# Optimization experiments

Hardware: AMD Instinct MI355X
Metric: run time of the kernel (lower is better)

The kernel has to match this reference:

```python
import jax, jax.numpy as jnp
import numpy as np

NHEAD = 16
D_MODEL = 1024
D_K = D_MODEL // NHEAD


def setup_inputs() -> dict:
    key = jax.random.key(0)
    ks = jax.random.split(key, 12)
    B, S, D = 2, 2048, D_MODEL
    scale = 1.0 / np.sqrt(D)
    inp = {
        "value": jax.random.normal(ks[0], (B, S, D), dtype=jnp.float32),
        "key": jax.random.normal(ks[1], (B, S, D), dtype=jnp.float32),
        "query": jax.random.normal(ks[2], (B, S, D), dtype=jnp.float32),
        "mask": jax.random.randint(ks[3], (B, 1, S, S), 0, 2, dtype=jnp.int32),
        "Wv": jax.random.normal(ks[4], (D, D), dtype=jnp.float32) * scale,
        "bv": jnp.zeros((D,), dtype=jnp.float32),
        "Wk": jax.random.normal(ks[5], (D, D), dtype=jnp.float32) * scale,
        "bk": jnp.zeros((D,), dtype=jnp.float32),
        "Wq": jax.random.normal(ks[6], (D, D), dtype=jnp.float32) * scale,
        "bq": jnp.zeros((D,), dtype=jnp.float32),
        "Wo": jax.random.normal(ks[7], (D, D), dtype=jnp.float32) * scale,
        "bo": jnp.zeros((D,), dtype=jnp.float32),
    }
    return inp


def reference(value, key, query, mask, Wv, bv, Wk, bk, Wq, bq, Wo, bo):
    B, S, D = value.shape
    H, Dk = NHEAD, D_K

    def proj(x, W, b):
        # nn.Linear: x @ W^T + b, then split heads -> [B, H, S, Dk]
        return (x @ W.T + b).reshape(B, S, H, Dk).transpose(0, 2, 1, 3)

    v = proj(value, Wv, bv)
    k = proj(key, Wk, bk)
    q = proj(query, Wq, bq)

    # NOTE: source code swaps K and V when calling attention():
    #   scores = Q @ V^T / sqrt(d_k);  out = softmax(scores) @ K
    scores = jnp.einsum("bhqd,bhkd->bhqk", q, v) / jnp.sqrt(jnp.float32(Dk))
    scores = jnp.where(mask == 0, jnp.float32(-1e9), scores)
    attn = jax.nn.softmax(scores, axis=-1)  # [B, H, S, S]
    attr_value = jnp.einsum("bhqk,bhkd->bhqd", attn, k)

    out = attr_value.transpose(0, 2, 1, 3).reshape(B, S, H * Dk)
    return out @ Wo.T + bo
```

## Files before the change

### kernel.cpp

```cpp
#include <hip/hip_runtime.h>

#define S_LEN 2048
#define DMODEL 1024
#define NHEADS 16
#define DKH 64

typedef __attribute__((ext_vector_type(8))) short bf16x8;
typedef __attribute__((ext_vector_type(4))) short bf16x4;
typedef __attribute__((ext_vector_type(4))) float f32x4;

#if __has_builtin(__builtin_amdgcn_exp2f)
#define EXP2F(x) __builtin_amdgcn_exp2f(x)
#define QSCALE (0.125f * 1.44269504f)
#else
#define EXP2F(x) __expf(x)
#define QSCALE 0.125f
#endif

static __device__ __forceinline__ short f2bf(float f) {
    unsigned b = __float_as_uint(f);
    b = (b + 0x7FFFu + ((b >> 16) & 1u)) >> 16;
    return (short)b;
}

static __device__ __forceinline__ unsigned pktrunc(float lo, float hi) {
#if __has_builtin(__builtin_amdgcn_perm)
    return __builtin_amdgcn_perm(__float_as_uint(hi), __float_as_uint(lo), 0x07060302u);
#else
    return (__float_as_uint(lo) >> 16) | (__float_as_uint(hi) & 0xFFFF0000u);
#endif
}

static __device__ __forceinline__ f32x4 mfma16(bf16x8 a, bf16x8 b, f32x4 c) {
    return __builtin_amdgcn_mfma_f32_16x16x32_bf16(a, b, c, 0, 0, 0);
}

static __device__ __forceinline__ f32x4 mfma_k16(bf16x4 a, bf16x4 b, f32x4 c) {
    return __builtin_amdgcn_mfma_f32_16x16x16bf16_1k(a, b, c, 0, 0, 0);
}

static __device__ __forceinline__ void glds16(const short* g, short* l) {
    __builtin_amdgcn_global_load_lds(
        (const __attribute__((address_space(1))) void*)g,
        (__attribute__((address_space(3))) void*)l, 16, 0, 0);
}

struct CvtArgs { const float* src[7]; short* dst[7]; };

__global__ __launch_bounds__(256) void prep(CvtArgs a, const int* __restrict__ mask,
                                            unsigned long long* __restrict__ mw) {
    if (blockIdx.x < 8192) {
        const size_t i8 = ((size_t)blockIdx.x * 256 + threadIdx.x) * 8;
        int seg; size_t off;
        if (i8 < ((size_t)12 << 20)) { seg = (int)(i8 >> 22); off = i8 & ((1u << 22) - 1); }
        else { size_t r = i8 - ((size_t)12 << 20); seg = 3 + (int)(r >> 20); off = r & ((1u << 20) - 1); }
        const float* s = a.src[seg] + off;
        float4 x0 = *(const float4*)s, x1 = *(const float4*)(s + 4);
        short o[8];
        o[0] = f2bf(x0.x); o[1] = f2bf(x0.y); o[2] = f2bf(x0.z); o[3] = f2bf(x0.w);
        o[4] = f2bf(x1.x); o[5] = f2bf(x1.y); o[6] = f2bf(x1.z); o[7] = f2bf(x1.w);
        *(uint4*)(a.dst[seg] + off) = *(uint4*)o;
    } else {
        const int wv = ((blockIdx.x - 8192) << 2) + (threadIdx.x >> 6);
        const int lane = threadIdx.x & 63;
        const size_t base = (size_t)wv << 4;
        #pragma unroll 4
        for (int it = 0; it < 16; ++it) {
            const size_t w = base + it;
            const int m = mask[(w << 6) + lane];
            unsigned long long bal = __ballot(m != 0);
            if (lane == 0) mw[w] = bal;
        }
    }
}

struct GemmArgs { const short* X[3]; const short* W[3]; const float* B[3];
                  void* C[3]; float scale[3]; };

template <int MODE>
__global__ __launch_bounds__(256) void gemm_bt(GemmArgs a) {
    __shared__ short Ah[128 * 32];
    __shared__ short Bh[128 * 32];
    const int z = blockIdx.z;
    const short* X = a.X[z];
    const short* W = a.W[z];
    const float* bias = a.B[z];
    const float scl = a.scale[z];

    const int t = threadIdx.x, wid = t >> 6, lane = t & 63;
    const int l15 = lane & 15, lq = lane >> 4;
    int m0, n0;
    if (MODE == 0 && z == 2) { m0 = blockIdx.y << 7; n0 = blockIdx.x << 7; }
    else                     { m0 = blockIdx.x << 7; n0 = blockIdx.y << 7; }
    const int wm = (wid >> 1) << 6, wn = (wid & 1) << 6;

    const int kb = (lane & 3) ^ ((lane >> 3) & 3);
    const int r0 = (wid << 5) + (lane >> 2);
    const short* ag0 = X + (size_t)(m0 + r0) * 1024 + (kb << 3);
    const short* ag1 = ag0 + 16 * 1024;
    const short* bg0 = W + (size_t)(n0 + r0) * 1024 + (kb << 3);
    const short* bg1 = bg0 + 16 * 1024;
    short* lA0 = Ah + (wid << 5) * 32;
    short* lA1 = lA0 + 16 * 32;
    short* lB0 = Bh + (wid << 5) * 32;
    short* lB1 = lB0 + 16 * 32;

    const int fpos = (lq ^ ((l15 >> 1) & 3)) << 3;

    f32x4 acc[4][4] = {};

    for (int k0 = 0; k0 < 1024; k0 += 32) {
        __syncthreads();
        glds16(ag0, lA0); glds16(ag1, lA1);
        glds16(bg0, lB0); glds16(bg1, lB1);
        ag0 += 32; ag1 += 32; bg0 += 32; bg1 += 32;
        __syncthreads();

        bf16x8 af[4], bfr[4];
        #pragma unroll
        for (int i = 0; i < 4; ++i)
            af[i] = *(const bf16x8*)&Ah[(wm + i * 16 + l15) * 32 + fpos];
        #pragma unroll
        for (int j = 0; j < 4; ++j)
            bfr[j] = *(const bf16x8*)&Bh[(wn + j * 16 + l15) * 32 + fpos];
        #pragma unroll
        for (int i = 0; i < 4; ++i)
            #pragma unroll
            for (int j = 0; j < 4; ++j)
                acc[i][j] = mfma16(af[i], bfr[j], acc[i][j]);
    }

    if (MODE == 0 && z == 2) {
        #pragma unroll
        for (int i = 0; i < 4; ++i) {
            #pragma unroll
            for (int r = 0; r < 4; ++r) {
                const int o = m0 + wm + i * 16 + (lq << 2) + r;
                const float bo_ = bias[o];
                const int h = o >> 6, d = o & 63;
                #pragma unroll
                for (int j = 0; j < 4; ++j) {
                    const int n = n0 + wn + j * 16 + l15;
                    const int bb = n >> 11, s = n & 2047;
                    ((short*)a.C[2])[(((size_t)((bb * 16 + h) << 6) + d) << 11) + s] =
                        f2bf(acc[i][j][r] + bo_);
                }
            }
        }
        return;
    }

    #pragma unroll
    for (int j = 0; j < 4; ++j) {
        const int n = n0 + wn + j * 16 + l15;
        const float bn = bias[n];
        #pragma unroll
        for (int i = 0; i < 4; ++i) {
            const int mbase = m0 + wm + i * 16 + (lq << 2);
            #pragma unroll
            for (int r = 0; r < 4; ++r) {
                const float val = (acc[i][j][r] + bn) * scl;
                const int m = mbase + r;
                if (MODE == 0) {
                    const int b = m >> 11, s = m & 2047, h = n >> 6, d = n & 63;
                    ((short*)a.C[z])[((((size_t)(b * 16 + h)) << 11) + s) * 64 + d] = f2bf(val);
                } else {
                    ((float*)a.C[z])[((size_t)m << 10) + n] = val;
                }
            }
        }
    }
}

__global__ __launch_bounds__(256, 4) void attn4(
    const short* __restrict__ Qh, const short* __restrict__ Vh,
    const short* __restrict__ Kt, const unsigned long long* __restrict__ MW,
    short* __restrict__ Opart, float* __restrict__ lpart)
{
    __shared__ short Vs[64 * 64];
    __shared__ short Ks[64 * 64];

    const int t = threadIdx.x, wid = t >> 6, lane = t & 63;
    const int l15 = lane & 15, lq = lane >> 4;
    const int bh = blockIdx.y, b = bh >> 4;
    const int z = blockIdx.z;
    const int ib = (blockIdx.x << 7) + (wid << 5);
    const int jbase = z << 10;

    bf16x8 qf[2][2];
    #pragma unroll
    for (int it = 0; it < 2; ++it) {
        const short* qp = Qh + ((size_t)bh * 2048 + ib + it * 16 + l15) * 64 + (lq << 3);
        qf[it][0] = *(const bf16x8*)qp;
        qf[it][1] = *(const bf16x8*)(qp + 32);
    }

    const int sr = lane >> 3, pc = lane & 7;
    const int lc = pc ^ sr;
    const int wr = wid << 4;
    const short* vsrc = Vh + (size_t)bh * 131072 + (size_t)(jbase + wr + sr) * 64 + (lc << 3);
    const short* ksrc = Kt + (size_t)bh * 131072 + (size_t)(wr + sr) * 2048 + jbase + (lc << 3);
    short* vdst = Vs + (wr << 6);
    short* kdst = Ks + (wr << 6);

    const unsigned long long* mwp0 = MW + ((size_t)b * 2048 + ib + l15) * 32 + (z << 4);
    const unsigned long long* mwp1 = mwp0 + (size_t)16 * 32;

    const int x7 = l15 & 7;
    int voff[2], koff[4];
    #pragma unroll
    for (int p = 0; p < 2; ++p) voff[p] = (((p << 2) + lq) ^ x7) << 3;
    #pragma unroll
    for (int jt = 0; jt < 4; ++jt) {
        const int c8 = (jt << 2) + lq;
        koff[jt] = (((c8 >> 1) ^ x7) << 3) + ((c8 & 1) << 2);
    }

    f32x4 O[2][4] = {};
    f32x4 lsum[2] = {};
    bf16x4 ones;
    #pragma unroll
    for (int e = 0; e < 4; ++e) ones[e] = (short)0x3F80;

    for (int jc = 0; jc < 16; ++jc) {
        __syncthreads();
        glds16(vsrc, vdst);
        glds16(vsrc + 512, vdst + 512);
        glds16(ksrc, kdst);
        glds16(ksrc + 8 * 2048, kdst + 512);
        vsrc += 4096; ksrc += 64;

        uint2 mword[2];
        mword[0] = *(const uint2*)(mwp0 + jc);
        mword[1] = *(const uint2*)(mwp1 + jc);
        __syncthreads();

        bf16x8 vf[4][2];
        #pragma unroll
        for (int jt = 0; jt < 4; ++jt) {
            const short* vp = &Vs[((jt << 4) + l15) << 6];
            vf[jt][0] = *(const bf16x8*)(vp + voff[0]);
            vf[jt][1] = *(const bf16x8*)(vp + voff[1]);
        }

        bf16x4 paf[2][4];
        #pragma unroll
        for (int it = 0; it < 2; ++it) {
            const unsigned wx = mword[it].x, wy = mword[it].y;
            #pragma unroll
            for (int jt = 0; jt < 4; ++jt) {
                f32x4 sc = {};
                sc = mfma16(vf[jt][0], qf[it][0], sc);
                sc = mfma16(vf[jt][1], qf[it][1], sc);
                const unsigned w32 = (jt < 2) ? wx : wy;
                float p[4];
                #pragma unroll
                for (int r = 0; r < 4; ++r) {
                    const unsigned bit = (w32 >> (((jt & 1) << 4) + (lq << 2) + r)) & 1u;
                    const float e = EXP2F(sc[r]);
                    p[r] = bit ? e : 0.f;
                }
                uint2 uu;
                uu.x = pktrunc(p[0], p[1]);
                uu.y = pktrunc(p[2], p[3]);
                paf[it][jt] = __builtin_bit_cast(bf16x4, uu);
                lsum[it] = mfma_k16(paf[it][jt], ones, lsum[it]);
            }
        }

        #pragma unroll
        for (int dt = 0; dt < 4; ++dt) {
            const short* kp = &Ks[((dt << 4) + l15) << 6];
            #pragma unroll
            for (int jt = 0; jt < 4; ++jt) {
                const bf16x4 kfv = *(const bf16x4*)(kp + koff[jt]);
                O[0][dt] = mfma_k16(paf[0][jt], kfv, O[0][dt]);
                O[1][dt] = mfma_k16(paf[1][jt], kfv, O[1][dt]);
            }
        }
    }

    const size_t zb = (size_t)((z << 5) + bh) * 2048;
    #pragma unroll
    for (int it = 0; it < 2; ++it) {
        const int rb = ib + (it << 4) + (lq << 2);
        if (l15 == 0) {
            #pragma unroll
            for (int r = 0; r < 4; ++r)
                lpart[zb + rb + r] = lsum[it][r];
        }
        #pragma unroll
        for (int dt = 0; dt < 4; ++dt)
            #pragma unroll
            for (int r = 0; r < 4; ++r)
                Opart[(zb + rb + r) * 64 + (dt << 4) + l15] = f2bf(O[it][dt][r]);
    }
}

__global__ __launch_bounds__(256) void combine(const short* __restrict__ Op,
                                               const float* __restrict__ lp,
                                               short* __restrict__ attr) {
    const int idx = blockIdx.x * 256 + threadIdx.x;
    const int d8 = (idx & 7) << 3;
    const int srow = (idx >> 3) & 2047;
    const int bh = idx >> 14, b = bh >> 4, h = bh & 15;
    const size_t r0 = (size_t)bh * 2048 + srow;
    const size_t r1 = r0 + (size_t)32 * 2048;
    uint4 a = *(const uint4*)(Op + r0 * 64 + d8);
    uint4 c = *(const uint4*)(Op + r1 * 64 + d8);
    const float inv = 1.f / (lp[r0] + lp[r1]);
    const unsigned* au = (const unsigned*)&a;
    const unsigned* cu = (const unsigned*)&c;
    short o[8];
    #pragma unroll
    for (int i = 0; i < 4; ++i) {
        const float a0 = __uint_as_float(au[i] << 16);
        const float a1 = __uint_as_float(au[i] & 0xFFFF0000u);
        const float c0 = __uint_as_float(cu[i] << 16);
        const float c1 = __uint_as_float(cu[i] & 0xFFFF0000u);
        o[2 * i + 0] = f2bf((a0 + c0) * inv);
        o[2 * i + 1] = f2bf((a1 + c1) * inv);
    }
    *(uint4*)&attr[((size_t)b * 2048 + srow) * 1024 + (h << 6) + d8] = *(uint4*)o;
}

extern "C" void kernel_launch(void* const* d_in, const int* in_sizes, int n_in,
                              void* d_out, int out_size, void* d_ws, size_t ws_size,
                              hipStream_t stream) {
    const float* value = (const float*)d_in[0];
    const float* key   = (const float*)d_in[1];
    const float* query = (const float*)d_in[2];
    const int*   mask  = (const int*)d_in[3];
    const float* bv = (const float*)d_in[5];
    const float* bk = (const float*)d_in[7];
    const float* bq = (const float*)d_in[9];
    const float* bo = (const float*)d_in[11];
    float* out = (float*)d_out;

    const size_t M1 = (size_t)1 << 20, M4 = (size_t)1 << 22;
    short* ws = (short*)d_ws;
    short* Xq = ws;
    short* Xk = ws + M4;
    short* Xv = ws + 2 * M4;
    short* Wc0 = ws + 3 * M4;
    short* Wc1 = Wc0 + M1;
    short* Wc2 = Wc1 + M1;
    short* Wc3 = Wc2 + M1;
    short* qh = ws + 4 * M4;
    short* kt = ws + 5 * M4;
    short* vh = ws + 6 * M4;
    unsigned long long* maskw = (unsigned long long*)(ws + 7 * M4);
    short* attr = Xq;
    short* Opart = Xk;
    float* lpart = (float*)Wc0;

    CvtArgs cv;
    cv.src[0] = query; cv.dst[0] = Xq;
    cv.src[1] = key;   cv.dst[1] = Xk;
    cv.src[2] = value; cv.dst[2] = Xv;
    cv.src[3] = (const float*)d_in[8];  cv.dst[3] = Wc0;
    cv.src[4] = (const float*)d_in[6];  cv.dst[4] = Wc1;
    cv.src[5] = (const float*)d_in[4];  cv.dst[5] = Wc2;
    cv.src[6] = (const float*)d_in[10]; cv.dst[6] = Wc3;
    prep<<<10240, 256, 0, stream>>>(cv, mask, maskw);

    GemmArgs g1;
    g1.X[0] = Xq;  g1.W[0] = Wc0; g1.B[0] = bq; g1.C[0] = qh; g1.scale[0] = QSCALE;
    g1.X[1] = Xv;  g1.W[1] = Wc2; g1.B[1] = bv; g1.C[1] = vh; g1.scale[1] = 1.f;
    g1.X[2] = Wc1; g1.W[2] = Xk;  g1.B[2] = bk; g1.C[2] = kt; g1.scale[2] = 1.f;
    gemm_bt<0><<<dim3(32, 8, 3), 256, 0, stream>>>(g1);

    attn4<<<dim3(16, 32, 2), 256, 0, stream>>>(qh, vh, kt, maskw, Opart, lpart);

    combine<<<2048, 256, 0, stream>>>(Opart, lpart, attr);

    GemmArgs g2;
    g2.X[0] = attr; g2.W[0] = Wc3; g2.B[0] = bo; g2.C[0] = out; g2.scale[0] = 1.f;
    g2.X[1] = attr; g2.W[1] = Wc3; g2.B[1] = bo; g2.C[1] = out; g2.scale[1] = 1.f;
    g2.X[2] = attr; g2.W[2] = Wc3; g2.B[2] = bo; g2.C[2] = out; g2.scale[2] = 1.f;
    gemm_bt<1><<<dim3(32, 8, 1), 256, 0, stream>>>(g2);
}
```

Measured before the change: 270.2 us.

## Double-buffer GEMM and attention LDS tiles, use K32 MFMA, smaller output GEMM tile

After: 275.7 us. 2.0% more time.

```diff
diff --git a/kernel.cpp b/kernel.cpp
--- a/kernel.cpp
+++ b/kernel.cpp
@@ -6,7 +6,6 @@
 #define DKH 64
 
 typedef __attribute__((ext_vector_type(8))) short bf16x8;
-typedef __attribute__((ext_vector_type(4))) short bf16x4;
 typedef __attribute__((ext_vector_type(4))) float f32x4;
 
 #if __has_builtin(__builtin_amdgcn_exp2f)
@@ -33,10 +32,6 @@
 
 static __device__ __forceinline__ f32x4 mfma16(bf16x8 a, bf16x8 b, f32x4 c) {
     return __builtin_amdgcn_mfma_f32_16x16x32_bf16(a, b, c, 0, 0, 0);
-}
-
-static __device__ __forceinline__ f32x4 mfma_k16(bf16x4 a, bf16x4 b, f32x4 c) {
-    return __builtin_amdgcn_mfma_f32_16x16x16bf16_1k(a, b, c, 0, 0, 0);
 }
 
 static __device__ __forceinline__ void glds16(const short* g, short* l) {
@@ -77,10 +72,10 @@
 struct GemmArgs { const short* X[3]; const short* W[3]; const float* B[3];
                   void* C[3]; float scale[3]; };
 
-template <int MODE>
+template <int MODE, int TM>
 __global__ __launch_bounds__(256) void gemm_bt(GemmArgs a) {
-    __shared__ short Ah[128 * 32];
-    __shared__ short Bh[128 * 32];
+    __shared__ short Ah[2][TM * 32];
+    __shared__ short Bh[2][128 * 32];
     const int z = blockIdx.z;
     const short* X = a.X[z];
     const short* W = a.W[z];
@@ -91,40 +86,61 @@
     const int l15 = lane & 15, lq = lane >> 4;
     int m0, n0;
     if (MODE == 0 && z == 2) { m0 = blockIdx.y << 7; n0 = blockIdx.x << 7; }
-    else                     { m0 = blockIdx.x << 7; n0 = blockIdx.y << 7; }
-    const int wm = (wid >> 1) << 6, wn = (wid & 1) << 6;
+    else { m0 = (TM == 128) ? (blockIdx.x << 7) : (blockIdx.x << 6); n0 = blockIdx.y << 7; }
+    constexpr int IT = (TM == 128) ? 4 : 2;
+    const int wm = (TM == 128) ? ((wid >> 1) << 6) : ((wid >> 1) << 5);
+    const int wn = (wid & 1) << 6;
 
     const int kb = (lane & 3) ^ ((lane >> 3) & 3);
-    const int r0 = (wid << 5) + (lane >> 2);
-    const short* ag0 = X + (size_t)(m0 + r0) * 1024 + (kb << 3);
-    const short* ag1 = ag0 + 16 * 1024;
-    const short* bg0 = W + (size_t)(n0 + r0) * 1024 + (kb << 3);
+    const short *ag0, *ag1 = nullptr;
+    int aoff0, aoff1 = 0;
+    if (TM == 128) {
+        const int r0 = (wid << 5) + (lane >> 2);
+        ag0 = X + (size_t)(m0 + r0) * 1024 + (kb << 3);
+        ag1 = ag0 + 16 * 1024;
+        aoff0 = (wid << 5) * 32;
+        aoff1 = aoff0 + 16 * 32;
+    } else {
+        const int r0 = (wid << 4) + (lane >> 2);
+        ag0 = X + (size_t)(m0 + r0) * 1024 + (kb << 3);
+        aoff0 = (wid << 4) * 32;
+    }
+    const int rb = (wid << 5) + (lane >> 2);
+    const short* bg0 = W + (size_t)(n0 + rb) * 1024 + (kb << 3);
     const short* bg1 = bg0 + 16 * 1024;
-    short* lA0 = Ah + (wid << 5) * 32;
-    short* lA1 = lA0 + 16 * 32;
-    short* lB0 = Bh + (wid << 5) * 32;
-    short* lB1 = lB0 + 16 * 32;
+    const int boff0 = (wid << 5) * 32, boff1 = boff0 + 16 * 32;
 
     const int fpos = (lq ^ ((l15 >> 1) & 3)) << 3;
 
-    f32x4 acc[4][4] = {};
-
-    for (int k0 = 0; k0 < 1024; k0 += 32) {
+    f32x4 acc[IT][4] = {};
+
+    glds16(ag0, Ah[0] + aoff0);
+    if (TM == 128) glds16(ag1, Ah[0] + aoff1);
+    glds16(bg0, Bh[0] + boff0);
+    glds16(bg1, Bh[0] + boff1);
+
+    for (int kc = 0; kc < 32; ++kc) {
         __syncthreads();
-        glds16(ag0, lA0); glds16(ag1, lA1);
-        glds16(bg0, lB0); glds16(bg1, lB1);
-        ag0 += 32; ag1 += 32; bg0 += 32; bg1 += 32;
-        __syncthreads();
-
-        bf16x8 af[4], bfr[4];
-        #pragma unroll
-        for (int i = 0; i < 4; ++i)
-            af[i] = *(const bf16x8*)&Ah[(wm + i * 16 + l15) * 32 + fpos];
+        if (kc < 31) {
+            const int nb = (kc + 1) & 1;
+            const int ko = (kc + 1) << 5;
+            glds16(ag0 + ko, Ah[nb] + aoff0);
+            if (TM == 128) glds16(ag1 + ko, Ah[nb] + aoff1);
+            glds16(bg0 + ko, Bh[nb] + boff0);
+            glds16(bg1 + ko, Bh[nb] + boff1);
+        }
+        const short* Ac = Ah[kc & 1];
+        const short* Bc = Bh[kc & 1];
+
+        bf16x8 af[IT], bfr[4];
+        #pragma unroll
+        for (int i = 0; i < IT; ++i)
+            af[i] = *(const bf16x8*)&Ac[(wm + i * 16 + l15) * 32 + fpos];
         #pragma unroll
         for (int j = 0; j < 4; ++j)
-            bfr[j] = *(const bf16x8*)&Bh[(wn + j * 16 + l15) * 32 + fpos];
-        #pragma unroll
-        for (int i = 0; i < 4; ++i)
+            bfr[j] = *(const bf16x8*)&Bc[(wn + j * 16 + l15) * 32 + fpos];
+        #pragma unroll
+        for (int i = 0; i < IT; ++i)
             #pragma unroll
             for (int j = 0; j < 4; ++j)
                 acc[i][j] = mfma16(af[i], bfr[j], acc[i][j]);
@@ -141,8 +157,11 @@
                 #pragma unroll
                 for (int j = 0; j < 4; ++j) {
                     const int n = n0 + wn + j * 16 + l15;
-                    const int bb = n >> 11, s = n & 2047;
-                    ((short*)a.C[2])[(((size_t)((bb * 16 + h) << 6) + d) << 11) + s] =
+                    const int bb = n >> 11;
+                    const int j5 = n & 31;
+                    const int kap = ((j5 >> 2) & 3) * 8 + ((j5 >> 4) & 1) * 4 + (j5 & 3);
+                    const int sp = (n & 2047 & ~31) | kap;
+                    ((short*)a.C[2])[(((size_t)((bb * 16 + h) << 6) + d) << 11) + sp] =
                         f2bf(acc[i][j][r] + bo_);
                 }
             }
@@ -155,7 +174,7 @@
         const int n = n0 + wn + j * 16 + l15;
         const float bn = bias[n];
         #pragma unroll
-        for (int i = 0; i < 4; ++i) {
+        for (int i = 0; i < IT; ++i) {
             const int mbase = m0 + wm + i * 16 + (lq << 2);
             #pragma unroll
             for (int r = 0; r < 4; ++r) {
@@ -172,13 +191,13 @@
     }
 }
 
-__global__ __launch_bounds__(256, 4) void attn4(
+__global__ __launch_bounds__(256, 4) void attn5(
     const short* __restrict__ Qh, const short* __restrict__ Vh,
     const short* __restrict__ Kt, const unsigned long long* __restrict__ MW,
     short* __restrict__ Opart, float* __restrict__ lpart)
 {
-    __shared__ short Vs[64 * 64];
-    __shared__ short Ks[64 * 64];
+    __shared__ short Vs[2][64 * 64];
+    __shared__ short Ks[2][64 * 64];
 
     const int t = threadIdx.x, wid = t >> 6, lane = t & 63;
     const int l15 = lane & 15, lq = lane >> 4;
@@ -200,53 +219,58 @@
     const int wr = wid << 4;
     const short* vsrc = Vh + (size_t)bh * 131072 + (size_t)(jbase + wr + sr) * 64 + (lc << 3);
     const short* ksrc = Kt + (size_t)bh * 131072 + (size_t)(wr + sr) * 2048 + jbase + (lc << 3);
-    short* vdst = Vs + (wr << 6);
-    short* kdst = Ks + (wr << 6);
+    const int sdst = (wr << 6);
 
     const unsigned long long* mwp0 = MW + ((size_t)b * 2048 + ib + l15) * 32 + (z << 4);
     const unsigned long long* mwp1 = mwp0 + (size_t)16 * 32;
 
     const int x7 = l15 & 7;
-    int voff[2], koff[4];
-    #pragma unroll
-    for (int p = 0; p < 2; ++p) voff[p] = (((p << 2) + lq) ^ x7) << 3;
-    #pragma unroll
-    for (int jt = 0; jt < 4; ++jt) {
-        const int c8 = (jt << 2) + lq;
-        koff[jt] = (((c8 >> 1) ^ x7) << 3) + ((c8 & 1) << 2);
-    }
+    int off[2];
+    #pragma unroll
+    for (int p = 0; p < 2; ++p) off[p] = (((p << 2) + lq) ^ x7) << 3;
 
     f32x4 O[2][4] = {};
     f32x4 lsum[2] = {};
-    bf16x4 ones;
-    #pragma unroll
-    for (int e = 0; e < 4; ++e) ones[e] = (short)0x3F80;
+    bf16x8 ones8;
+    #pragma unroll
+    for (int e = 0; e < 8; ++e) ones8[e] = (short)0x3F80;
+
+    glds16(vsrc, Vs[0] + sdst);
+    glds16(vsrc + 512, Vs[0] + sdst + 512);
+    glds16(ksrc, Ks[0] + sdst);
+    glds16(ksrc + 8 * 2048, Ks[0] + sdst + 512);
 
     for (int jc = 0; jc < 16; ++jc) {
         __syncthreads();
-        glds16(vsrc, vdst);
-        glds16(vsrc + 512, vdst + 512);
-        glds16(ksrc, kdst);
-        glds16(ksrc + 8 * 2048, kdst + 512);
-        vsrc += 4096; ksrc += 64;
+        if (jc < 15) {
+            const int nb = (jc + 1) & 1;
+            const short* v2 = vsrc + (size_t)(jc + 1) * 4096;
+            const short* k2 = ksrc + (jc + 1) * 64;
+            glds16(v2, Vs[nb] + sdst);
+            glds16(v2 + 512, Vs[nb] + sdst + 512);
+            glds16(k2, Ks[nb] + sdst);
+            glds16(k2 + 8 * 2048, Ks[nb] + sdst + 512);
+        }
+        const short* vbuf = Vs[jc & 1];
+        const short* kbuf = Ks[jc & 1];
 
         uint2 mword[2];
         mword[0] = *(const uint2*)(mwp0 + jc);
         mword[1] = *(const uint2*)(mwp1 + jc);
-        __syncthreads();
 
         bf16x8 vf[4][2];
         #pragma unroll
         for (int jt = 0; jt < 4; ++jt) {
-            const short* vp = &Vs[((jt << 4) + l15) << 6];
-            vf[jt][0] = *(const bf16x8*)(vp + voff[0]);
-            vf[jt][1] = *(const bf16x8*)(vp + voff[1]);
-        }
-
-        bf16x4 paf[2][4];
+            const short* vp = &vbuf[((jt << 4) + l15) << 6];
+            vf[jt][0] = *(const bf16x8*)(vp + off[0]);
+            vf[jt][1] = *(const bf16x8*)(vp + off[1]);
+        }
+
+        bf16x8 pa8[2][2];
         #pragma unroll
         for (int it = 0; it < 2; ++it) {
             const unsigned wx = mword[it].x, wy = mword[it].y;
+            uint2 uu[4];
             #pragma unroll
             for (int jt = 0; jt < 4; ++jt) {
                 f32x4 sc = {};
@@ -260,22 +284,27 @@
                     const float e = EXP2F(sc[r]);
                     p[r] = bit ? e : 0.f;
                 }
-                uint2 uu;
-                uu.x = pktrunc(p[0], p[1]);
-                uu.y = pktrunc(p[2], p[3]);
-                paf[it][jt] = __builtin_bit_cast(bf16x4, uu);
-                lsum[it] = mfma_k16(paf[it][jt], ones, lsum[it]);
+                uu[jt].x = pktrunc(p[0], p[1]);
+                uu[jt].y = pktrunc(p[2], p[3]);
             }
+            uint4 u0, u1;
+            u0.x = uu[0].x; u0.y = uu[0].y; u0.z = uu[1].x; u0.w = uu[1].y;
+            u1.x = uu[2].x; u1.y = uu[2].y; u1.z = uu[3].x; u1.w = uu[3].y;
+            pa8[it][0] = __builtin_bit_cast(bf16x8, u0);
+            pa8[it][1] = __builtin_bit_cast(bf16x8, u1);
+            lsum[it] = mfma16(pa8[it][0], ones8, lsum[it]);
+            lsum[it] = mfma16(pa8[it][1], ones8, lsum[it]);
         }
 
         #pragma unroll
         for (int dt = 0; dt < 4; ++dt) {
-            const short* kp = &Ks[((dt << 4) + l15) << 6];
-            #pragma unroll
-            for (int jt = 0; jt < 4; ++jt) {
-                const bf16x4 kfv = *(const bf16x4*)(kp + koff[jt]);
-                O[0][dt] = mfma_k16(paf[0][jt], kfv, O[0][dt]);
-                O[1][dt] = mfma_k16(paf[1][jt], kfv, O[1][dt]);
+            const short* kp = &kbuf[((dt << 4) + l15) << 6];
+            const bf16x8 kf0 = *(const bf16x8*)(kp + off[0]);
+            const bf16x8 kf1 = *(const bf16x8*)(kp + off[1]);
+            #pragma unroll
+            for (int it = 0; it < 2; ++it) {
+                O[it][dt] = mfma16(pa8[it][0], kf0, O[it][dt]);
+                O[it][dt] = mfma16(pa8[it][1], kf1, O[it][dt]);
             }
         }
     }
@@ -283,17 +312,17 @@
     const size_t zb = (size_t)((z << 5) + bh) * 2048;
     #pragma unroll
     for (int it = 0; it < 2; ++it) {
-        const int rb = ib + (it << 4) + (lq << 2);
+        const int rb2 = ib + (it << 4) + (lq << 2);
         if (l15 == 0) {
             #pragma unroll
             for (int r = 0; r < 4; ++r)
-                lpart[zb + rb + r] = lsum[it][r];
+                lpart[zb + rb2 + r] = lsum[it][r];
         }
         #pragma unroll
         for (int dt = 0; dt < 4; ++dt)
             #pragma unroll
             for (int r = 0; r < 4; ++r)
-                Opart[(zb + rb + r) * 64 + (dt << 4) + l15] = f2bf(O[it][dt][r]);
+                Opart[(zb + rb2 + r) * 64 + (dt << 4) + l15] = f2bf(O[it][dt][r]);
     }
 }
 
@@ -368,9 +397,9 @@
     g1.X[0] = Xq;  g1.W[0] = Wc0; g1.B[0] = bq; g1.C[0] = qh; g1.scale[0] = QSCALE;
     g1.X[1] = Xv;  g1.W[1] = Wc2; g1.B[1] = bv; g1.C[1] = vh; g1.scale[1] = 1.f;
     g1.X[2] = Wc1; g1.W[2] = Xk;  g1.B[2] = bk; g1.C[2] = kt; g1.scale[2] = 1.f;
-    gemm_bt<0><<<dim3(32, 8, 3), 256, 0, stream>>>(g1);
-
-    attn4<<<dim3(16, 32, 2), 256, 0, stream>>>(qh, vh, kt, maskw, Opart, lpart);
+    gemm_bt<0, 128><<<dim3(32, 8, 3), 256, 0, stream>>>(g1);
+
+    attn5<<<dim3(16, 32, 2), 256, 0, stream>>>(qh, vh, kt, maskw, Opart, lpart);
 
     combine<<<2048, 256, 0, stream>>>(Opart, lpart, attr);
 
@@ -378,5 +407,5 @@
     g2.X[0] = attr; g2.W[0] = Wc3; g2.B[0] = bo; g2.C[0] = out; g2.scale[0] = 1.f;
     g2.X[1] = attr; g2.W[1] = Wc3; g2.B[1] = bo; g2.C[1] = out; g2.scale[1] = 1.f;
     g2.X[2] = attr; g2.W[2] = Wc3; g2.B[2] = bo; g2.C[2] = out; g2.scale[2] = 1.f;
-    gemm_bt<1><<<dim3(32, 8, 1), 256, 0, stream>>>(g2);
-}
+    gemm_bt<1, 64><<<dim3(64, 8, 1), 256, 0, stream>>>(g2);
+}
```
